# Kernel optimization log

Measured on AMD Instinct MI355X. Metric: run time of the kernel, lower is better.

The kernel has to match this reference:

```python
import jax, jax.numpy as jnp
import numpy as np

N = 100000       # nodes
E = 3200000      # edges (avg degree 32)
NFEAT, NHID, NCLASS = 256, 128, 40


def setup_inputs() -> dict:
    key = jax.random.key(0)
    ks = jax.random.split(key, 6)
    x = jax.random.normal(ks[0], (N, NFEAT), jnp.float32)
    edge_rows = jax.random.randint(ks[1], (E,), 0, N)   # destination nodes
    edge_cols = jax.random.randint(ks[2], (E,), 0, N)   # source nodes
    # SageConv proj: Linear(2*in, out, bias=False); weight stored [out, in] torch-style
    W1 = jax.random.normal(ks[3], (NHID, 2 * NFEAT), jnp.float32) * 0.05
    W2 = jax.random.normal(ks[4], (NHID, 2 * NHID), jnp.float32) * 0.05
    mlp_W = jax.random.normal(ks[5], (NCLASS, NHID), jnp.float32) * 0.05  # init.normal_(std=0.05)
    mlp_b = jnp.zeros((NCLASS,), jnp.float32)
    return {"x": x, "W1": W1, "W2": W2, "mlp_W": mlp_W, "mlp_b": mlp_b,
            "edge_rows": edge_rows, "edge_cols": edge_cols}


def _sage_conv(h, W, rows, cols, deg):
    # neigh = spmm(adj, h) / (deg + 1); adj binary COO (rows <- cols)
    neigh = jax.ops.segment_sum(h[cols], rows, num_segments=N) / (deg + 1.0)[:, None]
    return jnp.concatenate([h, neigh], axis=-1) @ W.T


def reference(x, W1, W2, mlp_W, mlp_b, edge_rows, edge_cols):
    deg = jax.ops.segment_sum(jnp.ones((E,), x.dtype), edge_rows, num_segments=N)
    h = jax.nn.relu(_sage_conv(x, W1, edge_rows, edge_cols, deg))   # dropout: eval no-op
    h = jax.nn.relu(_sage_conv(h, W2, edge_rows, edge_cols, deg))
    logits = h @ mlp_W.T + mlp_b
    return jax.nn.log_softmax(logits, axis=1)
```

## Files before the change

kernel.cpp:

```cpp
#include <hip/hip_runtime.h>
#include <hip/hip_bf16.h>

#define NFEAT 256
#define NHID  128
#define NCLASS 40

typedef __attribute__((ext_vector_type(8))) short short8;
typedef __attribute__((ext_vector_type(4))) float float4v;

__device__ __forceinline__ unsigned short f2bf(float f) {
    union { float f; unsigned u; } v; v.f = f;
    unsigned r = v.u + 0x7fff + ((v.u >> 16) & 1);
    return (unsigned short)(r >> 16);
}
__device__ __forceinline__ float bflo(unsigned u) { return __uint_as_float(u << 16); }
__device__ __forceinline__ float bfhi(unsigned u) { return __uint_as_float(u & 0xffff0000u); }
__device__ __forceinline__ unsigned cvtpk_bf16(float a, float b) {
    unsigned r;
    asm("v_cvt_pk_bf16_f32 %0, %1, %2" : "=v"(r) : "v"(a), "v"(b));
    return r;
}

__device__ __forceinline__ void ld_g2l16(const unsigned short* gp, unsigned short* lp) {
    __builtin_amdgcn_global_load_lds((const __attribute__((address_space(1))) unsigned short*)gp,
                                     (__attribute__((address_space(3))) unsigned short*)lp,
                                     16, 0, 0);
}

#define TILE_E 4096
#define WCAP   20480

__global__ __launch_bounds__(256) void bin_scatter(const int* __restrict__ rows,
                                                   const int* __restrict__ cols,
                                                   int* __restrict__ gcur,
                                                   unsigned* __restrict__ binned, int E, int nbuck) {
    __shared__ int hh[256];
    __shared__ int lbase[256];
    __shared__ int lcur[256];
    int t = threadIdx.x;
    hh[t] = 0;
    __syncthreads();
    int e0 = blockIdx.x * TILE_E;
    int4 rv[4];
    #pragma unroll
    for (int it = 0; it < TILE_E / 1024; ++it) {
        int base = e0 + (it * 256 + t) * 4;
        if (base + 3 < E) {
            rv[it] = *reinterpret_cast<const int4*>(&rows[base]);
            atomicAdd(&hh[rv[it].x >> 9], 1);
            atomicAdd(&hh[rv[it].y >> 9], 1);
            atomicAdd(&hh[rv[it].z >> 9], 1);
            atomicAdd(&hh[rv[it].w >> 9], 1);
        } else {
            for (int k = 0; k < 4; ++k)
                if (base + k < E) atomicAdd(&hh[rows[base + k] >> 9], 1);
        }
    }
    __syncthreads();
    if (t < nbuck) {
        int h = hh[t];
        lbase[t] = t * WCAP + (h ? atomicAdd(&gcur[t], h) : 0);
        lcur[t] = 0;
    }
    __syncthreads();
    #pragma unroll
    for (int it = 0; it < TILE_E / 1024; ++it) {
        int base = e0 + (it * 256 + t) * 4;
        if (base + 3 < E) {
            int4 r = rv[it];
            int4 c = *reinterpret_cast<const int4*>(&cols[base]);
            int b0 = r.x >> 9, b1 = r.y >> 9, b2 = r.z >> 9, b3 = r.w >> 9;
            int d0 = lbase[b0] + atomicAdd(&lcur[b0], 1);
            int d1 = lbase[b1] + atomicAdd(&lcur[b1], 1);
            int d2 = lbase[b2] + atomicAdd(&lcur[b2], 1);
            int d3 = lbase[b3] + atomicAdd(&lcur[b3], 1);
            binned[d0] = ((unsigned)(r.x & 511) << 17) | (unsigned)c.x;
            binned[d1] = ((unsigned)(r.y & 511) << 17) | (unsigned)c.y;
            binned[d2] = ((unsigned)(r.z & 511) << 17) | (unsigned)c.z;
            binned[d3] = ((unsigned)(r.w & 511) << 17) | (unsigned)c.w;
        } else {
            for (int k = 0; k < 4; ++k)
                if (base + k < E) {
                    int r = rows[base + k];
                    int b = r >> 9;
                    int dst = lbase[b] + atomicAdd(&lcur[b], 1);
                    binned[dst] = ((unsigned)(r & 511) << 17) | (unsigned)cols[base + k];
                }
        }
    }
}

__global__ __launch_bounds__(256) void fill_win(const unsigned* __restrict__ binned,
                                                const int* __restrict__ gcur,
                                                int4* __restrict__ rpd,
                                                int* __restrict__ csr_cols, int N) {
    __shared__ int h[512];
    __shared__ int ps[256];
    __shared__ int lcur[512];
    int t = threadIdx.x;
    int w = blockIdx.x;
    int r0 = w << 9;
    h[t] = 0; h[t + 256] = 0;
    __syncthreads();
    int beg = w * WCAP, end = beg + gcur[w];
    for (int e = beg + t; e < end; e += 256)
        atomicAdd(&h[binned[e] >> 17], 1);
    __syncthreads();
    int pair = h[2 * t] + h[2 * t + 1];
    ps[t] = pair;
    __syncthreads();
    for (int off = 1; off < 256; off <<= 1) {
        int tmp = (t >= off) ? ps[t - off] : 0;
        __syncthreads();
        ps[t] += tmp;
        __syncthreads();
    }
    int base0 = beg + ps[t] - pair;
    int base1 = base0 + h[2 * t];
    int r_a = r0 + 2 * t, r_b = r0 + 2 * t + 1;
    if (r_a < N) {
        int4 m; m.x = base0; m.y = h[2 * t];
        m.z = __float_as_int(1.0f / ((float)h[2 * t] + 1.0f)); m.w = 0;
        rpd[r_a] = m;
    }
    if (r_b < N) {
        int4 m; m.x = base1; m.y = h[2 * t + 1];
        m.z = __float_as_int(1.0f / ((float)h[2 * t + 1] + 1.0f)); m.w = 0;
        rpd[r_b] = m;
    }
    lcur[2 * t] = base0;
    lcur[2 * t + 1] = base1;
    __syncthreads();
    for (int e = beg + t; e < end; e += 256) {
        unsigned v = binned[e];
        int idx = atomicAdd(&lcur[v >> 17], 1);
        csr_cols[idx] = (int)(v & 0x1FFFFu);
    }
}

__global__ __launch_bounds__(256) void repack_all(const float* __restrict__ W1,
                                                  const float* __restrict__ W2,
                                                  const float* __restrict__ Wm,
                                                  unsigned short* __restrict__ Wp1,
                                                  unsigned short* __restrict__ Wp2,
                                                  unsigned short* __restrict__ Wb) {
    int b = blockIdx.x, t = threadIdx.x;
    if (b < 256) {
        float v = (b < 128) ? W1[b * 512 + t] : W1[(b - 128) * 512 + 256 + t];
        Wp1[(size_t)(t >> 5) * 256 * 32 + b * 32 + (t & 31)] = f2bf(v);
    } else if (b < 512) {
        int o = b - 256;
        if (t < 128) {
            float v = (o < 128) ? W2[o * 256 + t] : W2[(o - 128) * 256 + 128 + t];
            Wp2[(size_t)(t >> 5) * 256 * 32 + o * 32 + (t & 31)] = f2bf(v);
        }
    } else {
        int o = b - 512;
        if (t < 128) Wb[o * 128 + t] = (o < NCLASS) ? f2bf(Wm[o * 128 + t]) : 0;
    }
}

__global__ __launch_bounds__(512) void gemm1_mfma(const float* __restrict__ X,
                                                  const unsigned short* __restrict__ Wp,
                                                  unsigned short* __restrict__ PS,
                                                  unsigned char* __restrict__ PN8,
                                                  int M) {
    __shared__ unsigned short sA[128 * 32];
    __shared__ unsigned short sB[256 * 32];
    const int t    = threadIdx.x;
    const int lane = t & 63;
    const int wave = t >> 6;
    const int m0 = blockIdx.x * 128;
    const int wm = (wave >> 2) * 64;
    const int wn = (wave & 3) * 64;

    const int r15 = lane & 15;
    const int k8  = (lane >> 4) * 8;
    const int arow = t >> 2;
    const int ac8  = (t & 3) * 8;
    const int brow = lane >> 2;
    const int bc8  = (lane & 3) * 8;

    float4v acc[4][4] = {{{0.f,0.f,0.f,0.f}}};
    const int gm = min(m0 + arow, M - 1);
    const float* gA = X + (size_t)gm * 256 + ac8;

    for (int k0 = 0; k0 < 256; k0 += 32) {
        const unsigned short* pan = Wp + (size_t)(k0 >> 5) * 256 * 32;
        float4 v0 = *reinterpret_cast<const float4*>(gA + k0);
        float4 v1 = *reinterpret_cast<const float4*>(gA + k0 + 4);
        uint4 q;
        q.x = cvtpk_bf16(v0.x, v0.y);
        q.y = cvtpk_bf16(v0.z, v0.w);
        q.z = cvtpk_bf16(v1.x, v1.y);
        q.w = cvtpk_bf16(v1.z, v1.w);
        *reinterpret_cast<uint4*>(&sA[arow * 32 + ac8]) = q;
        #pragma unroll
        for (int it = 0; it < 2; ++it) {
            int slab = it * 128 + wave * 16;
            ld_g2l16(pan + (size_t)(slab + brow) * 32 + bc8, &sB[slab * 32]);
        }
        __syncthreads();

        short8 aF[4], bF[4];
        #pragma unroll
        for (int i = 0; i < 4; ++i)
            aF[i] = *reinterpret_cast<const short8*>(&sA[(wm + i * 16 + r15) * 32 + k8]);
        #pragma unroll
        for (int j = 0; j < 4; ++j)
            bF[j] = *reinterpret_cast<const short8*>(&sB[(wn + j * 16 + r15) * 32 + k8]);
        #pragma unroll
        for (int i = 0; i < 4; ++i)
            #pragma unroll
            for (int j = 0; j < 4; ++j)
                acc[i][j] = __builtin_amdgcn_mfma_f32_16x16x32_bf16(aF[i], bF[j], acc[i][j], 0, 0, 0);
        __syncthreads();
    }

    #pragma unroll
    for (int i = 0; i < 4; ++i) {
        #pragma unroll
        for (int r = 0; r < 4; ++r) {
            int row = m0 + wm + i * 16 + (lane >> 4) * 4 + r;
            #pragma unroll
            for (int j = 0; j < 4; ++j) {
                float v  = acc[i][j][r];
                float vn = __shfl_xor(v, 1);
                int cN = wn + j * 16 + r15;
                if (row < M && !(r15 & 1)) {
                    if (cN < 128) {
                        *reinterpret_cast<unsigned*>(&PS[(size_t)row * 128 + cN]) = cvtpk_bf16(v, vn);
                    } else {
                        unsigned p8 = __builtin_amdgcn_cvt_pk_fp8_f32(v, vn, 0u, false);
                        *reinterpret_cast<unsigned short*>(&PN8[(size_t)row * 128 + (cN - 128)]) =
                            (unsigned short)p8;
                    }
                }
            }
        }
    }
}

__global__ __launch_bounds__(512) void gemm2_mfma(const unsigned short* __restrict__ H,
                                                  const unsigned short* __restrict__ Wp,
                                                  unsigned short* __restrict__ PS,
                                                  unsigned char* __restrict__ PN8,
                                                  int M) {
    __shared__ unsigned short sA[128 * 32];
    __shared__ unsigned short sB[256 * 32];
    const int t    = threadIdx.x;
    const int lane = t & 63;
    const int wave = t >> 6;
    const int m0 = blockIdx.x * 128;
    const int wm = (wave >> 2) * 64;
    const int wn = (wave & 3) * 64;

    const int r15 = lane & 15;
    const int k8  = (lane >> 4) * 8;
    const int brow = lane >> 2;
    const int bc8  = (lane & 3) * 8;

    float4v acc[4][4] = {{{0.f,0.f,0.f,0.f}}};

    for (int k0 = 0; k0 < 128; k0 += 32) {
        const unsigned short* pan = Wp + (size_t)(k0 >> 5) * 256 * 32;
        int slabA = wave * 16;
        ld_g2l16(H + (size_t)(m0 + slabA + brow) * 128 + k0 + bc8, &sA[slabA * 32]);
        #pragma unroll
        for (int it = 0; it < 2; ++it) {
            int slab = it * 128 + wave * 16;
            ld_g2l16(pan + (size_t)(slab + brow) * 32 + bc8, &sB[slab * 32]);
        }
        __syncthreads();

        short8 aF[4], bF[4];
        #pragma unroll
        for (int i = 0; i < 4; ++i)
            aF[i] = *reinterpret_cast<const short8*>(&sA[(wm + i * 16 + r15) * 32 + k8]);
        #pragma unroll
        for (int j = 0; j < 4; ++j)
            bF[j] = *reinterpret_cast<const short8*>(&sB[(wn + j * 16 + r15) * 32 + k8]);
        #pragma unroll
        for (int i = 0; i < 4; ++i)
            #pragma unroll
            for (int j = 0; j < 4; ++j)
                acc[i][j] = __builtin_amdgcn_mfma_f32_16x16x32_bf16(aF[i], bF[j], acc[i][j], 0, 0, 0);
        __syncthreads();
    }

    #pragma unroll
    for (int i = 0; i < 4; ++i) {
        #pragma unroll
        for (int r = 0; r < 4; ++r) {
            int row = m0 + wm + i * 16 + (lane >> 4) * 4 + r;
            #pragma unroll
            for (int j = 0; j < 4; ++j) {
                float v  = acc[i][j][r];
                float vn = __shfl_xor(v, 1);
                int cN = wn + j * 16 + r15;
                if (row < M && !(r15 & 1)) {
                    if (cN < 128) {
                        *reinterpret_cast<unsigned*>(&PS[(size_t)row * 128 + cN]) = cvtpk_bf16(v, vn);
                    } else {
                        unsigned p8 = __builtin_amdgcn_cvt_pk_fp8_f32(v, vn, 0u, false);
                        *reinterpret_cast<unsigned short*>(&PN8[(size_t)row * 128 + (cN - 128)]) =
                            (unsigned short)p8;
                    }
                }
            }
        }
    }
}

__device__ __forceinline__ void acc_fp8x8(uint2 u,
                                          float& a0, float& a1, float& a2, float& a3,
                                          float& a4, float& a5, float& a6, float& a7) {
    auto f01 = __builtin_amdgcn_cvt_pk_f32_fp8(u.x, false);
    auto f23 = __builtin_amdgcn_cvt_pk_f32_fp8(u.x, true);
    auto f45 = __builtin_amdgcn_cvt_pk_f32_fp8(u.y, false);
    auto f67 = __builtin_amdgcn_cvt_pk_f32_fp8(u.y, true);
    a0 += f01[0]; a1 += f01[1]; a2 += f23[0]; a3 += f23[1];
    a4 += f45[0]; a5 += f45[1]; a6 += f67[0]; a7 += f67[1];
}

__global__ __launch_bounds__(256) void gather_combine(const unsigned short* __restrict__ PS,
                                                      const unsigned char* __restrict__ PN8,
                                                      const int4* __restrict__ rpd,
                                                      const int* __restrict__ csr_cols,
                                                      unsigned short* __restrict__ H, int N) {
    int node = (blockIdx.x * blockDim.x + threadIdx.x) >> 6;
    if (node >= N) return;
    int lane = threadIdx.x & 63;
    int grp  = lane >> 4;
    int l16  = lane & 15;
    int4 md = rpd[node];
    int beg = md.x, end = md.x + md.y;
    float id = __int_as_float(md.z);

    uint4 us = {0u, 0u, 0u, 0u};
    if (grp == 0)
        us = *reinterpret_cast<const uint4*>(&PS[(size_t)node * 128 + l16 * 8]);

    float a0=0,a1=0,a2=0,a3=0,a4=0,a5=0,a6=0,a7=0;
    int p0 = beg + grp;
    for (; p0 + 12 < end; p0 += 16) {
        int cA = csr_cols[p0];
        int cB = csr_cols[p0 + 4];
        int cC = csr_cols[p0 + 8];
        int cD = csr_cols[p0 + 12];
        uint2 uA = *reinterpret_cast<const uint2*>(&PN8[(size_t)cA * 128 + l16 * 8]);
        uint2 uB = *reinterpret_cast<const uint2*>(&PN8[(size_t)cB * 128 + l16 * 8]);
        uint2 uC = *reinterpret_cast<const uint2*>(&PN8[(size_t)cC * 128 + l16 * 8]);
        uint2 uD = *reinterpret_cast<const uint2*>(&PN8[(size_t)cD * 128 + l16 * 8]);
        acc_fp8x8(uA, a0, a1, a2, a3, a4, a5, a6, a7);
        acc_fp8x8(uB, a0, a1, a2, a3, a4, a5, a6, a7);
        acc_fp8x8(uC, a0, a1, a2, a3, a4, a5, a6, a7);
        acc_fp8x8(uD, a0, a1, a2, a3, a4, a5, a6, a7);
    }
    for (; p0 < end; p0 += 4) {
        int c = csr_cols[p0];
        uint2 u = *reinterpret_cast<const uint2*>(&PN8[(size_t)c * 128 + l16 * 8]);
        acc_fp8x8(u, a0, a1, a2, a3, a4, a5, a6, a7);
    }
    a0 += __shfl_xor(a0, 16); a1 += __shfl_xor(a1, 16);
    a2 += __shfl_xor(a2, 16); a3 += __shfl_xor(a3, 16);
    a4 += __shfl_xor(a4, 16); a5 += __shfl_xor(a5, 16);
    a6 += __shfl_xor(a6, 16); a7 += __shfl_xor(a7, 16);
    a0 += __shfl_xor(a0, 32); a1 += __shfl_xor(a1, 32);
    a2 += __shfl_xor(a2, 32); a3 += __shfl_xor(a3, 32);
    a4 += __shfl_xor(a4, 32); a5 += __shfl_xor(a5, 32);
    a6 += __shfl_xor(a6, 32); a7 += __shfl_xor(a7, 32);

    if (grp == 0) {
        float h0 = fmaxf(fmaf(a0, id, bflo(us.x)), 0.f);
        float h1 = fmaxf(fmaf(a1, id, bfhi(us.x)), 0.f);
        float h2 = fmaxf(fmaf(a2, id, bflo(us.y)), 0.f);
        float h3 = fmaxf(fmaf(a3, id, bfhi(us.y)), 0.f);
        float h4 = fmaxf(fmaf(a4, id, bflo(us.z)), 0.f);
        float h5 = fmaxf(fmaf(a5, id, bfhi(us.z)), 0.f);
        float h6 = fmaxf(fmaf(a6, id, bflo(us.w)), 0.f);
        float h7 = fmaxf(fmaf(a7, id, bfhi(us.w)), 0.f);
        uint4 o;
        o.x = cvtpk_bf16(h0, h1); o.y = cvtpk_bf16(h2, h3);
        o.z = cvtpk_bf16(h4, h5); o.w = cvtpk_bf16(h6, h7);
        *reinterpret_cast<uint4*>(&H[(size_t)node * 128 + l16 * 8]) = o;
    }
}

__global__ __launch_bounds__(256) void mlp_head_mfma(const unsigned short* __restrict__ H,
                                                     const unsigned short* __restrict__ Wb,
                                                     const float* __restrict__ bm,
                                                     float* __restrict__ out, int N) {
    __shared__ unsigned short sW[48 * 128];
    int t = threadIdx.x;
    for (int i = t; i < 48 * 128 / 2; i += 256)
        ((unsigned*)sW)[i] = ((const unsigned*)Wb)[i];
    __syncthreads();

    const int wave = t >> 6, lane = t & 63;
    const int m0 = blockIdx.x * 64 + wave * 16;
    if (m0 >= N) return;
    const int r15 = lane & 15;
    const int k8  = (lane >> 4) * 8;
    const int arow = min(m0 + r15, N - 1);

    float4v acc[3] = {{0.f,0.f,0.f,0.f},{0.f,0.f,0.f,0.f},{0.f,0.f,0.f,0.f}};
    #pragma unroll
    for (int k0 = 0; k0 < 128; k0 += 32) {
        short8 a = *reinterpret_cast<const short8*>(&H[(size_t)arow * 128 + k0 + k8]);
        #pragma unroll
        for (int f = 0; f < 3; ++f) {
            short8 b = *reinterpret_cast<const short8*>(&sW[(f * 16 + r15) * 128 + k0 + k8]);
            acc[f] = __builtin_amdgcn_mfma_f32_16x16x32_bf16(a, b, acc[f], 0, 0, 0);
        }
    }

    float bias[3]; bool cv[3];
    #pragma unroll
    for (int f = 0; f < 3; ++f) {
        int c = f * 16 + r15;
        cv[f] = (c < NCLASS);
        bias[f] = cv[f] ? bm[c] : 0.f;
    }
    #pragma unroll
    for (int r = 0; r < 4; ++r) {
        int node = m0 + (lane >> 4) * 4 + r;
        float lg[3];
        float m = -1e30f;
        #pragma unroll
        for (int f = 0; f < 3; ++f) {
            lg[f] = cv[f] ? (acc[f][r] + bias[f]) : -1e30f;
            m = fmaxf(m, lg[f]);
        }
        m = fmaxf(m, __shfl_xor(m, 1));
        m = fmaxf(m, __shfl_xor(m, 2));
        m = fmaxf(m, __shfl_xor(m, 4));
        m = fmaxf(m, __shfl_xor(m, 8));
        float s = 0.f;
        #pragma unroll
        for (int f = 0; f < 3; ++f) s += cv[f] ? __expf(lg[f] - m) : 0.f;
        s += __shfl_xor(s, 1);
        s += __shfl_xor(s, 2);
        s += __shfl_xor(s, 4);
        s += __shfl_xor(s, 8);
        float ls = __logf(s);
        if (node < N) {
            #pragma unroll
            for (int f = 0; f < 3; ++f)
                if (cv[f]) out[(size_t)node * NCLASS + f * 16 + r15] = lg[f] - m - ls;
        }
    }
}

extern "C" void kernel_launch(void* const* d_in, const int* in_sizes, int n_in,
                              void* d_out, int out_size, void* d_ws, size_t ws_size,
                              hipStream_t stream) {
    const float* x    = (const float*)d_in[0];
    const float* W1   = (const float*)d_in[1];
    const float* W2   = (const float*)d_in[2];
    const float* mlpW = (const float*)d_in[3];
    const float* mlpb = (const float*)d_in[4];
    const int*   rows = (const int*)d_in[5];
    const int*   cols = (const int*)d_in[6];

    const int N = in_sizes[0] / NFEAT;
    const int E = in_sizes[5];

    char* ws = (char*)d_ws;
    size_t off = 0;
    auto alloc = [&](size_t bytes) -> void* {
        void* p = ws + off;
        off = (off + bytes + 255) & ~(size_t)255;
        return p;
    };
    const int nbuck = (N + 511) >> 9;
    const int nblk  = (E + TILE_E - 1) / TILE_E;

    unsigned short* PS  = (unsigned short*)alloc((size_t)N * 128 * 2);
    unsigned char*  PN8 = (unsigned char*) alloc((size_t)N * 128);
    unsigned short* H   = (unsigned short*)alloc((size_t)N * 128 * 2);
    int4*  RPD    = (int4*) alloc((size_t)N * 16);
    int*   CSRC   = (int*)  alloc((size_t)nbuck * WCAP * 4);
    unsigned* BINNED = (unsigned*)alloc((size_t)nbuck * WCAP * 4);
    int*   GCUR   = (int*)  alloc((size_t)256 * 4);
    unsigned short* Wp1 = (unsigned short*)alloc((size_t)256 * 256 * 2);
    unsigned short* Wp2 = (unsigned short*)alloc((size_t)128 * 256 * 2);
    unsigned short* Wb  = (unsigned short*)alloc((size_t)48 * 128 * 2);

    hipMemsetAsync(GCUR, 0, 256 * 4, stream);
    bin_scatter<<<nblk, 256, 0, stream>>>(rows, cols, GCUR, BINNED, E, nbuck);
    fill_win<<<nbuck, 256, 0, stream>>>(BINNED, GCUR, RPD, CSRC, N);

    repack_all<<<560, 256, 0, stream>>>(W1, W2, mlpW, Wp1, Wp2, Wb);

    const int mblocks = (N + 127) / 128;
    const int gblocks = (int)(((long long)N * 64 + 255) / 256);

    gemm1_mfma<<<mblocks, 512, 0, stream>>>(x, Wp1, PS, PN8, N);
    gather_combine<<<gblocks, 256, 0, stream>>>(PS, PN8, RPD, CSRC, H, N);

    gemm2_mfma<<<mblocks, 512, 0, stream>>>(H, Wp2, PS, PN8, N);
    gather_combine<<<gblocks, 256, 0, stream>>>(PS, PN8, RPD, CSRC, H, N);

    mlp_head_mfma<<<(N + 63) / 64, 256, 0, stream>>>(H, Wb, mlpb, (float*)d_out, N);
}
```

Before: 447.7 us.

## Merge weight repack into binning kernel and CSR fill into first GEMM

Appends the weight repacking blocks to the edge-binning launch and runs the per-window CSR fill as extra leading blocks of the first GEMM launch. This cuts two kernel launches and lets the independent work overlap inside one grid instead of running back to back. The CSR fill is adapted to 512-thread blocks with guarded scan lanes. GEMM blocks now share a larger union shared buffer, which may affect occupancy, and the fill blocks may be scheduled unevenly next to GEMM tiles.

```diff
diff --git a/kernel.cpp b/kernel.cpp
--- a/kernel.cpp
+++ b/kernel.cpp
@@ -30,14 +30,38 @@
 #define TILE_E 4096
 #define WCAP   20480
 
-__global__ __launch_bounds__(256) void bin_scatter(const int* __restrict__ rows,
-                                                   const int* __restrict__ cols,
-                                                   int* __restrict__ gcur,
-                                                   unsigned* __restrict__ binned, int E, int nbuck) {
+__global__ __launch_bounds__(256) void prep_fused(const int* __restrict__ rows,
+                                                  const int* __restrict__ cols,
+                                                  int* __restrict__ gcur,
+                                                  unsigned* __restrict__ binned, int E, int nbuck,
+                                                  int nblk,
+                                                  const float* __restrict__ W1,
+                                                  const float* __restrict__ W2,
+                                                  const float* __restrict__ Wm,
+                                                  unsigned short* __restrict__ Wp1,
+                                                  unsigned short* __restrict__ Wp2,
+                                                  unsigned short* __restrict__ Wb) {
+    int t = threadIdx.x;
+    if ((int)blockIdx.x >= nblk) {
+        int b = blockIdx.x - nblk;
+        if (b < 256) {
+            float v = (b < 128) ? W1[b * 512 + t] : W1[(b - 128) * 512 + 256 + t];
+            Wp1[(size_t)(t >> 5) * 256 * 32 + b * 32 + (t & 31)] = f2bf(v);
+        } else if (b < 512) {
+            int o = b - 256;
+            if (t < 128) {
+                float v = (o < 128) ? W2[o * 256 + t] : W2[(o - 128) * 256 + 128 + t];
+                Wp2[(size_t)(t >> 5) * 256 * 32 + o * 32 + (t & 31)] = f2bf(v);
+            }
+        } else {
+            int o = b - 512;
+            if (t < 128) Wb[o * 128 + t] = (o < NCLASS) ? f2bf(Wm[o * 128 + t]) : 0;
+        }
+        return;
+    }
     __shared__ int hh[256];
     __shared__ int lbase[256];
     __shared__ int lcur[256];
-    int t = threadIdx.x;
     hh[t] = 0;
     __syncthreads();
     int e0 = blockIdx.x * TILE_E;
@@ -90,87 +114,71 @@
     }
 }
 
-__global__ __launch_bounds__(256) void fill_win(const unsigned* __restrict__ binned,
+__global__ __launch_bounds__(512) void gemm1_fw(const float* __restrict__ X,
+                                                const unsigned short* __restrict__ Wp,
+                                                unsigned short* __restrict__ PS,
+                                                unsigned char* __restrict__ PN8,
+                                                int M, int nfw,
+                                                const unsigned* __restrict__ binned,
                                                 const int* __restrict__ gcur,
                                                 int4* __restrict__ rpd,
                                                 int* __restrict__ csr_cols, int N) {
-    __shared__ int h[512];
-    __shared__ int ps[256];
-    __shared__ int lcur[512];
-    int t = threadIdx.x;
-    int w = blockIdx.x;
-    int r0 = w << 9;
-    h[t] = 0; h[t + 256] = 0;
-    __syncthreads();
-    int beg = w * WCAP, end = beg + gcur[w];
-    for (int e = beg + t; e < end; e += 256)
-        atomicAdd(&h[binned[e] >> 17], 1);
-    __syncthreads();
-    int pair = h[2 * t] + h[2 * t + 1];
-    ps[t] = pair;
-    __syncthreads();
-    for (int off = 1; off < 256; off <<= 1) {
-        int tmp = (t >= off) ? ps[t - off] : 0;
-        __syncthreads();
-        ps[t] += tmp;
-        __syncthreads();
-    }
-    int base0 = beg + ps[t] - pair;
-    int base1 = base0 + h[2 * t];
-    int r_a = r0 + 2 * t, r_b = r0 + 2 * t + 1;
-    if (r_a < N) {
-        int4 m; m.x = base0; m.y = h[2 * t];
-        m.z = __float_as_int(1.0f / ((float)h[2 * t] + 1.0f)); m.w = 0;
-        rpd[r_a] = m;
-    }
-    if (r_b < N) {
-        int4 m; m.x = base1; m.y = h[2 * t + 1];
-        m.z = __float_as_int(1.0f / ((float)h[2 * t + 1] + 1.0f)); m.w = 0;
-        rpd[r_b] = m;
-    }
-    lcur[2 * t] = base0;
-    lcur[2 * t + 1] = base1;
-    __syncthreads();
-    for (int e = beg + t; e < end; e += 256) {
-        unsigned v = binned[e];
-        int idx = atomicAdd(&lcur[v >> 17], 1);
-        csr_cols[idx] = (int)(v & 0x1FFFFu);
-    }
-}
-
-__global__ __launch_bounds__(256) void repack_all(const float* __restrict__ W1,
-                                                  const float* __restrict__ W2,
-                                                  const float* __restrict__ Wm,
-                                                  unsigned short* __restrict__ Wp1,
-                                                  unsigned short* __restrict__ Wp2,
-                                                  unsigned short* __restrict__ Wb) {
-    int b = blockIdx.x, t = threadIdx.x;
-    if (b < 256) {
-        float v = (b < 128) ? W1[b * 512 + t] : W1[(b - 128) * 512 + 256 + t];
-        Wp1[(size_t)(t >> 5) * 256 * 32 + b * 32 + (t & 31)] = f2bf(v);
-    } else if (b < 512) {
-        int o = b - 256;
-        if (t < 128) {
-            float v = (o < 128) ? W2[o * 256 + t] : W2[(o - 128) * 256 + 128 + t];
-            Wp2[(size_t)(t >> 5) * 256 * 32 + o * 32 + (t & 31)] = f2bf(v);
-        }
-    } else {
-        int o = b - 512;
-        if (t < 128) Wb[o * 128 + t] = (o < NCLASS) ? f2bf(Wm[o * 128 + t]) : 0;
-    }
-}
-
-__global__ __launch_bounds__(512) void gemm1_mfma(const float* __restrict__ X,
-                                                  const unsigned short* __restrict__ Wp,
-                                                  unsigned short* __restrict__ PS,
-                                                  unsigned char* __restrict__ PN8,
-                                                  int M) {
-    __shared__ unsigned short sA[128 * 32];
-    __shared__ unsigned short sB[256 * 32];
-    const int t    = threadIdx.x;
+    __shared__ __align__(16) char smem[24576];
+    const int t = threadIdx.x;
+
+    if ((int)blockIdx.x < nfw) {
+        int* h    = (int*)smem;
+        int* ps   = h + 512;
+        int* lcur = ps + 256;
+        int w = blockIdx.x;
+        int r0 = w << 9;
+        h[t] = 0;
+        if (t < 256) ps[t] = 0;
+        __syncthreads();
+        int beg = w * WCAP, end = beg + gcur[w];
+        for (int e = beg + t; e < end; e += 512)
+            atomicAdd(&h[binned[e] >> 17], 1);
+        __syncthreads();
+        int pair = 0;
+        if (t < 256) { pair = h[2 * t] + h[2 * t + 1]; ps[t] = pair; }
+        __syncthreads();
+        for (int off = 1; off < 256; off <<= 1) {
+            int tmp = (t >= off && t < 256) ? ps[t - off] : 0;
+            __syncthreads();
+            if (t < 256) ps[t] += tmp;
+            __syncthreads();
+        }
+        if (t < 256) {
+            int base0 = beg + ps[t] - pair;
+            int base1 = base0 + h[2 * t];
+            int r_a = r0 + 2 * t, r_b = r0 + 2 * t + 1;
+            if (r_a < N) {
+                int4 m; m.x = base0; m.y = h[2 * t];
+                m.z = __float_as_int(1.0f / ((float)h[2 * t] + 1.0f)); m.w = 0;
+                rpd[r_a] = m;
+            }
+            if (r_b < N) {
+                int4 m; m.x = base1; m.y = h[2 * t + 1];
+                m.z = __float_as_int(1.0f / ((float)h[2 * t + 1] + 1.0f)); m.w = 0;
+                rpd[r_b] = m;
+            }
+            lcur[2 * t] = base0;
+            lcur[2 * t + 1] = base1;
+        }
+        __syncthreads();
+        for (int e = beg + t; e < end; e += 512) {
+            unsigned v = binned[e];
+            int idx = atomicAdd(&lcur[v >> 17], 1);
+            csr_cols[idx] = (int)(v & 0x1FFFFu);
+        }
+        return;
+    }
+
+    unsigned short* sA = (unsigned short*)smem;
+    unsigned short* sB = (unsigned short*)(smem + 8192);
     const int lane = t & 63;
     const int wave = t >> 6;
-    const int m0 = blockIdx.x * 128;
+    const int m0 = (blockIdx.x - nfw) * 128;
     const int wm = (wave >> 2) * 64;
     const int wn = (wave & 3) * 64;
 
@@ -487,16 +495,15 @@
     unsigned short* Wp2 = (unsigned short*)alloc((size_t)128 * 256 * 2);
     unsigned short* Wb  = (unsigned short*)alloc((size_t)48 * 128 * 2);
 
-    hipMemsetAsync(GCUR, 0, 256 * 4, stream);
-    bin_scatter<<<nblk, 256, 0, stream>>>(rows, cols, GCUR, BINNED, E, nbuck);
-    fill_win<<<nbuck, 256, 0, stream>>>(BINNED, GCUR, RPD, CSRC, N);
-
-    repack_all<<<560, 256, 0, stream>>>(W1, W2, mlpW, Wp1, Wp2, Wb);
-
     const int mblocks = (N + 127) / 128;
     const int gblocks = (int)(((long long)N * 64 + 255) / 256);
 
-    gemm1_mfma<<<mblocks, 512, 0, stream>>>(x, Wp1, PS, PN8, N);
+    hipMemsetAsync(GCUR, 0, 256 * 4, stream);
+    prep_fused<<<nblk + 560, 256, 0, stream>>>(rows, cols, GCUR, BINNED, E, nbuck, nblk,
+                                               W1, W2, mlpW, Wp1, Wp2, Wb);
+
+    gemm1_fw<<<nbuck + mblocks, 512, 0, stream>>>(x, Wp1, PS, PN8, N, nbuck,
+                                                  BINNED, GCUR, RPD, CSRC, N);
     gather_combine<<<gblocks, 256, 0, stream>>>(PS, PN8, RPD, CSRC, H, N);
 
     gemm2_mfma<<<mblocks, 512, 0, stream>>>(H, Wp2, PS, PN8, N);
```

New measurement: 418.7 us. 1.07x faster.
